# Optimization experiments

Measured on AMD Instinct MI355X. Metric: run time of the kernel, lower is better.

## Reference

```python
import jax, jax.numpy as jnp
import numpy as np

N_ORDERS = 4  # edge groups processed sequentially by EmulsionConv


def setup_inputs() -> dict:
    key = jax.random.key(0)
    ks = jax.random.split(key, 12)
    N, E, D_IN, H, D_OUT, ED = 50000, 800000, 10, 64, 10, 1
    s = 0.1
    return {
        "x": jax.random.normal(ks[0], (N, D_IN), jnp.float32),
        "edge_index": jax.random.randint(ks[1], (2, E), 0, N, jnp.int32),
        "edge_features": jax.random.normal(ks[2], (E, ED), jnp.float32),
        "lin0_w": jax.random.normal(ks[3], (D_IN, H), jnp.float32) * s,
        "lin0_b": jnp.zeros((H,), jnp.float32),
        "lin1_w": jax.random.normal(ks[4], (H, H), jnp.float32) * s,
        "lin1_b": jnp.zeros((H,), jnp.float32),
        "lin2_w": jax.random.normal(ks[5], (H, H), jnp.float32) * s,
        "lin2_b": jnp.zeros((H,), jnp.float32),
        "em_w": jax.random.normal(ks[6], (3, 2 * H + ED, H), jnp.float32) * s,
        "em_b": jnp.zeros((3, H), jnp.float32),
        "ec_w": jax.random.normal(ks[7], (3, 2 * H, H), jnp.float32) * s,
        "ec_b": jnp.zeros((3, H), jnp.float32),
        "out_w": jax.random.normal(ks[8], (H, D_OUT), jnp.float32) * s,
        "out_b": jnp.zeros((D_OUT,), jnp.float32),
    }


def _emulsion_conv(x, edge_index, edge_features, w, b):
    # Sequential per-order gather -> MLP message -> scatter-add; direction=0 (aggregate at source).
    N = x.shape[0]
    E = edge_index.shape[1]
    per = E // N_ORDERS
    for i in range(N_ORDERS):
        sl = slice(i * per, (i + 1) * per)
        src = edge_index[0, sl]
        dst = edge_index[1, sl]
        x_j = x[src]  # [per, H]
        x_i = x[dst]  # [per, H]
        msg = jnp.concatenate([x_i, x_j - x_i, edge_features[sl]], axis=1)
        msg = jax.nn.relu(msg @ w + b)
        agg = jax.ops.segment_sum(msg, src, num_segments=N)
        x = (x + agg) / 2.0
    return x


def _edge_conv(x, edge_index, w, b):
    # EdgeConv: nn([x_i, x_j - x_i]) with max aggregation at target nodes.
    N = x.shape[0]
    src, dst = edge_index[0], edge_index[1]
    x_i = x[dst]
    x_j = x[src]
    msg = jax.nn.relu(jnp.concatenate([x_i, x_j - x_i], axis=1) @ w + b)
    agg = jax.ops.segment_max(msg, dst, num_segments=N)
    return jnp.where(jnp.isfinite(agg), agg, 0.0)  # empty segments -> 0


def reference(x, edge_index, edge_features,
              lin0_w, lin0_b, lin1_w, lin1_b, lin2_w, lin2_b,
              em_w, em_b, ec_w, ec_b, out_w, out_b):
    lin_ws = [lin0_w, lin1_w, lin2_w]
    lin_bs = [lin0_b, lin1_b, lin2_b]
    for i in range(3):
        x = jax.nn.relu(x @ lin_ws[i] + lin_bs[i])
        x = _emulsion_conv(x, edge_index, edge_features, em_w[i], em_b[i])
    for i in range(3):
        x = _edge_conv(x, edge_index, ec_w[i], ec_b[i])
    return x @ out_w + out_b
```

## Files before the change

kernel.cpp:

```cpp
#include <hip/hip_runtime.h>
#include <hip/hip_fp16.h>


#define NN 50000
#define NE 800000
#define PER 200000
#define HD 64
#define NKEY 250112

#define NB_COUNT 3125
#define NB_LIN   782
#define NB_PREP  192

typedef _Float16 half8 __attribute__((ext_vector_type(8)));
typedef float float4v __attribute__((ext_vector_type(4)));

__global__ __launch_bounds__(256) void setup_kernel(
        const int* __restrict__ ei, int* __restrict__ cnt,
        uchar2* __restrict__ rank,
        const float* __restrict__ x_in, const float* __restrict__ lw0,
        const float* __restrict__ lb0, float* __restrict__ x,
        const float* __restrict__ em_w, const float* __restrict__ ec_w,
        _Float16* __restrict__ wh) {
    __shared__ float xs[64][11];
    int t = threadIdx.x;
    int b = blockIdx.x;
    if (b < NB_COUNT) {
        int e = b * 256 + t;
        if (e >= NE) return;
        int src = ei[e];
        int dst = ei[NE + e];
        int o = e / PER;
        int r1 = atomicAdd(&cnt[o * NN + src], 1);
        int r2 = atomicAdd(&cnt[4 * NN + dst], 1);
        rank[e] = make_uchar2((unsigned char)r1, (unsigned char)r2);
    } else if (b < NB_COUNT + NB_LIN) {
        int n0 = (b - NB_COUNT) * 64;
        for (int idx = t; idx < 64 * 10; idx += 256) {
            int n = idx / 10, k = idx - n * 10;
            int g = n0 + n;
            xs[n][k] = (g < NN) ? x_in[(size_t)g * 10 + k] : 0.f;
        }
        __syncthreads();
        int ng = t >> 4;
        int f0 = (t & 15) * 4;
        float acc[4][4] = {};
        for (int k = 0; k < 10; ++k) {
            float4 w4 = *(const float4*)&lw0[k * HD + f0];
            #pragma unroll
            for (int j = 0; j < 4; ++j) {
                float xv = xs[ng * 4 + j][k];
                acc[j][0] += xv * w4.x; acc[j][1] += xv * w4.y;
                acc[j][2] += xv * w4.z; acc[j][3] += xv * w4.w;
            }
        }
        float4 b4 = *(const float4*)&lb0[f0];
        #pragma unroll
        for (int j = 0; j < 4; ++j) {
            int g = n0 + ng * 4 + j;
            if (g < NN) {
                float4 o;
                o.x = fmaxf(acc[j][0] + b4.x, 0.f);
                o.y = fmaxf(acc[j][1] + b4.y, 0.f);
                o.z = fmaxf(acc[j][2] + b4.z, 0.f);
                o.w = fmaxf(acc[j][3] + b4.w, 0.f);
                *(float4*)&x[(size_t)g * HD + f0] = o;
            }
        }
    } else {
        int idx = (b - NB_COUNT - NB_LIN) * 256 + t;
        int mat = idx >> 12, pos = idx & 4095;
        int n = pos >> 6, k = pos & 63;
        float val;
        if (mat < 3)      { const float* B = em_w + mat * 129 * 64;     val = B[k*64+n] - B[(64+k)*64+n]; }
        else if (mat < 6) { const float* B = em_w + (mat-3) * 129 * 64; val = B[(64+k)*64+n]; }
        else if (mat < 9) { const float* B = ec_w + (mat-6) * 128 * 64; val = B[k*64+n] - B[(64+k)*64+n]; }
        else              { const float* B = ec_w + (mat-9) * 128 * 64; val = B[(64+k)*64+n]; }
        _Float16 h = (_Float16)val;
        _Float16 l = (_Float16)(val - (float)h);
        wh[(size_t)mat * 4096 + n * 64 + k] = h;
        wh[(size_t)(12 + mat) * 4096 + n * 64 + k] = l;
    }
}

__global__ __launch_bounds__(256) void scan_blk(
        const int* __restrict__ cnt, int* __restrict__ bsum) {
    __shared__ int s[256];
    int t = threadIdx.x;
    int i = blockIdx.x * 256 + t;
    int c = (i < NKEY) ? cnt[i] : 0;
    s[t] = c; __syncthreads();
    for (int d = 1; d < 256; d <<= 1) {
        int v = (t >= d) ? s[t - d] : 0;
        __syncthreads(); s[t] += v; __syncthreads();
    }
    if (t == 255) bsum[blockIdx.x] = s[255];
}

__global__ __launch_bounds__(1024) void scan_top(
        const int* __restrict__ bsum, int* __restrict__ bofs, int nb) {
    __shared__ int s[1024];
    int t = threadIdx.x;
    int c = (t < nb) ? bsum[t] : 0;
    s[t] = c; __syncthreads();
    for (int d = 1; d < 1024; d <<= 1) {
        int v = (t >= d) ? s[t - d] : 0;
        __syncthreads(); s[t] += v; __syncthreads();
    }
    if (t < nb) bofs[t] = s[t] - c;
}

__global__ __launch_bounds__(256) void scan_fin(
        const int* __restrict__ cnt, const int* __restrict__ bofs,
        int* __restrict__ ofs) {
    __shared__ int s[256];
    int t = threadIdx.x;
    int i = blockIdx.x * 256 + t;
    int c = (i < NKEY) ? cnt[i] : 0;
    s[t] = c; __syncthreads();
    for (int d = 1; d < 256; d <<= 1) {
        int v = (t >= d) ? s[t - d] : 0;
        __syncthreads(); s[t] += v; __syncthreads();
    }
    if (i < NKEY) ofs[i] = bofs[blockIdx.x] + s[t] - c;
}

__global__ __launch_bounds__(256) void fill_kernel(
        const int* __restrict__ ei, const float* __restrict__ ef,
        const int* __restrict__ ofs, const uchar2* __restrict__ rank,
        unsigned* __restrict__ em_val, int* __restrict__ ec_val) {
    int e = blockIdx.x * 256 + threadIdx.x;
    if (e >= NE) return;
    int src = ei[e];
    int dst = ei[NE + e];
    int o = e / PER;
    uchar2 r = rank[e];
    int p1 = ofs[o * NN + src] + r.x;
    unsigned short eb = __half_as_ushort(__float2half_rn(ef[e]));
    em_val[p1] = ((unsigned)dst << 16) | (unsigned)eb;
    int p2 = ofs[4 * NN + dst] + r.y - NE;
    ec_val[p2] = src;
}

template<int K>
__global__ __launch_bounds__(256) void lin_kernel(
        const float* __restrict__ xin,
        const float* __restrict__ W, const float* __restrict__ bias,
        float* __restrict__ xout) {
    __shared__ float xs[64][K + 1];
    int t = threadIdx.x;
    int n0 = blockIdx.x * 64;
    for (int idx = t; idx < 64 * K; idx += 256) {
        int n = idx / K, k = idx - n * K;
        int g = n0 + n;
        xs[n][k] = (g < NN) ? xin[(size_t)g * K + k] : 0.f;
    }
    __syncthreads();
    int ng = t >> 4;
    int f0 = (t & 15) * 4;
    float acc[4][4] = {};
    for (int k = 0; k < K; ++k) {
        float4 w4 = *(const float4*)&W[k * HD + f0];
        #pragma unroll
        for (int j = 0; j < 4; ++j) {
            float xv = xs[ng * 4 + j][k];
            acc[j][0] += xv * w4.x; acc[j][1] += xv * w4.y;
            acc[j][2] += xv * w4.z; acc[j][3] += xv * w4.w;
        }
    }
    float4 b4 = *(const float4*)&bias[f0];
    #pragma unroll
    for (int j = 0; j < 4; ++j) {
        int g = n0 + ng * 4 + j;
        if (g < NN) {
            float4 o;
            o.x = fmaxf(acc[j][0] + b4.x, 0.f);
            o.y = fmaxf(acc[j][1] + b4.y, 0.f);
            o.z = fmaxf(acc[j][2] + b4.z, 0.f);
            o.w = fmaxf(acc[j][3] + b4.w, 0.f);
            *(float4*)&xout[(size_t)g * HD + f0] = o;
        }
    }
}

__global__ __launch_bounds__(256) void uv_mfma(
        const float* __restrict__ x,
        const _Float16* __restrict__ Wuh, const _Float16* __restrict__ Wul,
        const _Float16* __restrict__ Wvh, const _Float16* __restrict__ Wvl,
        const float* __restrict__ bias,
        _Float16* __restrict__ u, _Float16* __restrict__ v) {
    __shared__ _Float16 xh[64 * 72], xl[64 * 72];
    __shared__ _Float16 wuh[64 * 72], wul[64 * 72];
    __shared__ _Float16 wvh[64 * 72], wvl[64 * 72];
    __shared__ _Float16 rp[4 * 16 * 72];
    int t = threadIdx.x;
    int n0 = blockIdx.x * 64;

    {
        int node = t >> 2, k0 = (t & 3) * 16;
        int g = n0 + node;
        float f[16];
        if (g < NN) {
            const float4* xr = (const float4*)&x[(size_t)g * HD + k0];
            *(float4*)&f[0] = xr[0]; *(float4*)&f[4] = xr[1];
            *(float4*)&f[8] = xr[2]; *(float4*)&f[12] = xr[3];
        } else {
            #pragma unroll
            for (int j = 0; j < 16; ++j) f[j] = 0.f;
        }
        half8 h0, h1, l0, l1;
        #pragma unroll
        for (int j = 0; j < 8; ++j) {
            _Float16 h = (_Float16)f[j];
            h0[j] = h; l0[j] = (_Float16)(f[j] - (float)h);
            _Float16 g2 = (_Float16)f[j + 8];
            h1[j] = g2; l1[j] = (_Float16)(f[j + 8] - (float)g2);
        }
        *(half8*)&xh[node * 72 + k0] = h0; *(half8*)&xh[node * 72 + k0 + 8] = h1;
        *(half8*)&xl[node * 72 + k0] = l0; *(half8*)&xl[node * 72 + k0 + 8] = l1;
    }
    {
        int n = t >> 2, c = (t & 3) * 16;
        *(half8*)&wuh[n * 72 + c]     = *(const half8*)&Wuh[n * 64 + c];
        *(half8*)&wuh[n * 72 + c + 8] = *(const half8*)&Wuh[n * 64 + c + 8];
        *(half8*)&wul[n * 72 + c]     = *(const half8*)&Wul[n * 64 + c];
        *(half8*)&wul[n * 72 + c + 8] = *(const half8*)&Wul[n * 64 + c + 8];
        *(half8*)&wvh[n * 72 + c]     = *(const half8*)&Wvh[n * 64 + c];
        *(half8*)&wvh[n * 72 + c + 8] = *(const half8*)&Wvh[n * 64 + c + 8];
        *(half8*)&wvl[n * 72 + c]     = *(const half8*)&Wvl[n * 64 + c];
        *(half8*)&wvl[n * 72 + c + 8] = *(const half8*)&Wvl[n * 64 + c + 8];
    }
    __syncthreads();

    int w = t >> 6, lane = t & 63;
    int quad = lane >> 4, l16 = lane & 15;
    int m0 = w * 16;
    half8 ah0 = *(half8*)&xh[(m0 + l16) * 72 + quad * 8];
    half8 ah1 = *(half8*)&xh[(m0 + l16) * 72 + 32 + quad * 8];
    half8 al0 = *(half8*)&xl[(m0 + l16) * 72 + quad * 8];
    half8 al1 = *(half8*)&xl[(m0 + l16) * 72 + 32 + quad * 8];

    float4v au[4], av[4];
    #pragma unroll
    for (int nt = 0; nt < 4; ++nt) {
        int n = nt * 16 + l16;
        half8 bh0 = *(half8*)&wuh[n * 72 + quad * 8];
        half8 bh1 = *(half8*)&wuh[n * 72 + 32 + quad * 8];
        half8 bl0 = *(half8*)&wul[n * 72 + quad * 8];
        half8 bl1 = *(half8*)&wul[n * 72 + 32 + quad * 8];
        float4v acc = {0.f, 0.f, 0.f, 0.f};
        acc = __builtin_amdgcn_mfma_f32_16x16x32_f16(ah0, bh0, acc, 0, 0, 0);
        acc = __builtin_amdgcn_mfma_f32_16x16x32_f16(ah1, bh1, acc, 0, 0, 0);
        acc = __builtin_amdgcn_mfma_f32_16x16x32_f16(al0, bh0, acc, 0, 0, 0);
        acc = __builtin_amdgcn_mfma_f32_16x16x32_f16(al1, bh1, acc, 0, 0, 0);
        acc = __builtin_amdgcn_mfma_f32_16x16x32_f16(ah0, bl0, acc, 0, 0, 0);
        acc = __builtin_amdgcn_mfma_f32_16x16x32_f16(ah1, bl1, acc, 0, 0, 0);
        au[nt] = acc;
        half8 ch0 = *(half8*)&wvh[n * 72 + quad * 8];
        half8 ch1 = *(half8*)&wvh[n * 72 + 32 + quad * 8];
        half8 cl0 = *(half8*)&wvl[n * 72 + quad * 8];
        half8 cl1 = *(half8*)&wvl[n * 72 + 32 + quad * 8];
        float4v accv = {0.f, 0.f, 0.f, 0.f};
        accv = __builtin_amdgcn_mfma_f32_16x16x32_f16(ah0, ch0, accv, 0, 0, 0);
        accv = __builtin_amdgcn_mfma_f32_16x16x32_f16(ah1, ch1, accv, 0, 0, 0);
        accv = __builtin_amdgcn_mfma_f32_16x16x32_f16(al0, ch0, accv, 0, 0, 0);
        accv = __builtin_amdgcn_mfma_f32_16x16x32_f16(al1, ch1, accv, 0, 0, 0);
        accv = __builtin_amdgcn_mfma_f32_16x16x32_f16(ah0, cl0, accv, 0, 0, 0);
        accv = __builtin_amdgcn_mfma_f32_16x16x32_f16(ah1, cl1, accv, 0, 0, 0);
        av[nt] = accv;
    }

    _Float16* rpw = &rp[w * 16 * 72];
    #pragma unroll
    for (int nt = 0; nt < 4; ++nt) {
        float bn = bias[nt * 16 + l16];
        #pragma unroll
        for (int r = 0; r < 4; ++r)
            rpw[(quad * 4 + r) * 72 + nt * 16 + l16] = (_Float16)(au[nt][r] + bn);
    }
    int mr = lane >> 2, cr = (lane & 3) * 16;
    int gr = n0 + m0 + mr;
    if (gr < NN) {
        *(half8*)&u[(size_t)gr * HD + cr]     = *(half8*)&rpw[mr * 72 + cr];
        *(half8*)&u[(size_t)gr * HD + cr + 8] = *(half8*)&rpw[mr * 72 + cr + 8];
    }
    #pragma unroll
    for (int nt = 0; nt < 4; ++nt) {
        #pragma unroll
        for (int r = 0; r < 4; ++r)
            rpw[(quad * 4 + r) * 72 + nt * 16 + l16] = (_Float16)(av[nt][r]);
    }
    if (gr < NN) {
        *(half8*)&v[(size_t)gr * HD + cr]     = *(half8*)&rpw[mr * 72 + cr];
        *(half8*)&v[(size_t)gr * HD + cr + 8] = *(half8*)&rpw[mr * 72 + cr + 8];
    }
}

__device__ __forceinline__ void load_h8(const __half* p, float* o) {
    float4 r = *(const float4*)p;
    __half2 h0 = *reinterpret_cast<__half2*>(&r.x);
    __half2 h1 = *reinterpret_cast<__half2*>(&r.y);
    __half2 h2 = *reinterpret_cast<__half2*>(&r.z);
    __half2 h3 = *reinterpret_cast<__half2*>(&r.w);
    float2 f0 = __half22float2(h0), f1 = __half22float2(h1);
    float2 f2 = __half22float2(h2), f3 = __half22float2(h3);
    o[0] = f0.x; o[1] = f0.y; o[2] = f1.x; o[3] = f1.y;
    o[4] = f2.x; o[5] = f2.y; o[6] = f3.x; o[7] = f3.y;
}

__global__ __launch_bounds__(256) void em_edge(
        const unsigned* __restrict__ em_val, const int* __restrict__ ofs,
        const __half* __restrict__ u, const __half* __restrict__ v,
        const float* __restrict__ we, float* __restrict__ x, int order) {
    int t = threadIdx.x;
    int node = blockIdx.x * 32 + (t >> 3);
    if (node >= NN) return;
    int f0 = (t & 7) * 8;
    int key = order * NN + node;
    int s0 = ofs[key], s1 = ofs[key + 1];
    float vn[8], wef[8], acc[8] = {};
    load_h8(&v[(size_t)node * HD + f0], vn);
    *(float4*)&wef[0] = *(const float4*)&we[f0];
    *(float4*)&wef[4] = *(const float4*)&we[f0 + 4];
    int p = s0;
    for (; p + 2 <= s1; p += 2) {
        unsigned e0 = em_val[p], e1 = em_val[p + 1];
        float u0[8], u1[8];
        load_h8(&u[(size_t)(e0 >> 16) * HD + f0], u0);
        load_h8(&u[(size_t)(e1 >> 16) * HD + f0], u1);
        float ef0 = __half2float(__ushort_as_half((unsigned short)(e0 & 0xffff)));
        float ef1 = __half2float(__ushort_as_half((unsigned short)(e1 & 0xffff)));
        #pragma unroll
        for (int j = 0; j < 8; ++j) {
            acc[j] += fmaxf(u0[j] + vn[j] + ef0 * wef[j], 0.f)
                    + fmaxf(u1[j] + vn[j] + ef1 * wef[j], 0.f);
        }
    }
    if (p < s1) {
        unsigned e0 = em_val[p];
        float u0[8];
        load_h8(&u[(size_t)(e0 >> 16) * HD + f0], u0);
        float ef0 = __half2float(__ushort_as_half((unsigned short)(e0 & 0xffff)));
        #pragma unroll
        for (int j = 0; j < 8; ++j)
            acc[j] += fmaxf(u0[j] + vn[j] + ef0 * wef[j], 0.f);
    }
    float xr[8];
    *(float4*)&xr[0] = *(const float4*)&x[(size_t)node * HD + f0];
    *(float4*)&xr[4] = *(const float4*)&x[(size_t)node * HD + f0 + 4];
    #pragma unroll
    for (int j = 0; j < 8; ++j) xr[j] = (xr[j] + acc[j]) * 0.5f;
    *(float4*)&x[(size_t)node * HD + f0] = *(float4*)&xr[0];
    *(float4*)&x[(size_t)node * HD + f0 + 4] = *(float4*)&xr[4];
}

__global__ __launch_bounds__(256) void ec_edge(
        const int* __restrict__ ec_val, const int* __restrict__ ofs,
        const __half* __restrict__ u, const __half* __restrict__ v,
        float* __restrict__ x) {
    int t = threadIdx.x;
    int node = blockIdx.x * 32 + (t >> 3);
    if (node >= NN) return;
    int f0 = (t & 7) * 8;
    int s0 = ofs[4 * NN + node] - NE, s1 = ofs[4 * NN + node + 1] - NE;
    float un[8], m[8] = {};
    load_h8(&u[(size_t)node * HD + f0], un);
    int p = s0;
    for (; p + 2 <= s1; p += 2) {
        int i0 = ec_val[p], i1 = ec_val[p + 1];
        float v0[8], v1[8];
        load_h8(&v[(size_t)i0 * HD + f0], v0);
        load_h8(&v[(size_t)i1 * HD + f0], v1);
        #pragma unroll
        for (int j = 0; j < 8; ++j)
            m[j] = fmaxf(m[j], fmaxf(un[j] + v0[j], un[j] + v1[j]));
    }
    if (p < s1) {
        int i0 = ec_val[p];
        float v0[8];
        load_h8(&v[(size_t)i0 * HD + f0], v0);
        #pragma unroll
        for (int j = 0; j < 8; ++j) m[j] = fmaxf(m[j], un[j] + v0[j]);
    }
    *(float4*)&x[(size_t)node * HD + f0] = *(float4*)&m[0];
    *(float4*)&x[(size_t)node * HD + f0 + 4] = *(float4*)&m[4];
}

__global__ __launch_bounds__(256) void ec_out(
        const int* __restrict__ ec_val, const int* __restrict__ ofs,
        const __half* __restrict__ u, const __half* __restrict__ v,
        const float* __restrict__ ow, const float* __restrict__ ob,
        float* __restrict__ out) {
    __shared__ float xs[32][72];
    int t = threadIdx.x;
    int nl = t >> 3;
    int node = blockIdx.x * 32 + nl;
    int f0 = (t & 7) * 8;
    float m[8] = {};
    if (node < NN) {
        int s0 = ofs[4 * NN + node] - NE, s1 = ofs[4 * NN + node + 1] - NE;
        float un[8];
        load_h8(&u[(size_t)node * HD + f0], un);
        int p = s0;
        for (; p + 2 <= s1; p += 2) {
            int i0 = ec_val[p], i1 = ec_val[p + 1];
            float v0[8], v1[8];
            load_h8(&v[(size_t)i0 * HD + f0], v0);
            load_h8(&v[(size_t)i1 * HD + f0], v1);
            #pragma unroll
            for (int j = 0; j < 8; ++j)
                m[j] = fmaxf(m[j], fmaxf(un[j] + v0[j], un[j] + v1[j]));
        }
        if (p < s1) {
            int i0 = ec_val[p];
            float v0[8];
            load_h8(&v[(size_t)i0 * HD + f0], v0);
            #pragma unroll
            for (int j = 0; j < 8; ++j) m[j] = fmaxf(m[j], un[j] + v0[j]);
        }
    }
    #pragma unroll
    for (int j = 0; j < 8; ++j) xs[nl][f0 + j] = m[j];
    __syncthreads();
    for (int idx = t; idx < 32 * 10; idx += 256) {
        int n = idx / 10, f = idx - n * 10;
        int g = blockIdx.x * 32 + n;
        if (g >= NN) continue;
        float acc = ob[f];
        #pragma unroll
        for (int k = 0; k < HD; ++k) acc += xs[n][k] * ow[k * 10 + f];
        out[(size_t)g * 10 + f] = acc;
    }
}

extern "C" void kernel_launch(void* const* d_in, const int* in_sizes, int n_in,
                              void* d_out, int out_size, void* d_ws, size_t ws_size,
                              hipStream_t stream) {
    const float* x_in  = (const float*)d_in[0];
    const int*   ei    = (const int*)d_in[1];
    const float* ef    = (const float*)d_in[2];
    const float* lw[3] = {(const float*)d_in[3], (const float*)d_in[5], (const float*)d_in[7]};
    const float* lb[3] = {(const float*)d_in[4], (const float*)d_in[6], (const float*)d_in[8]};
    const float* em_w  = (const float*)d_in[9];
    const float* em_b  = (const float*)d_in[10];
    const float* ec_w  = (const float*)d_in[11];
    const float* ec_b  = (const float*)d_in[12];
    const float* ow    = (const float*)d_in[13];
    const float* ob    = (const float*)d_in[14];
    float* out = (float*)d_out;

    char* wsb = (char*)d_ws;
    size_t off = 0;
    auto alloc = [&](size_t bytes) {
        void* p = wsb + off;
        off = (off + bytes + 255) & ~(size_t)255;
        return p;
    };
    float*     x      = (float*)alloc((size_t)NN * HD * 4);
    _Float16*  u      = (_Float16*)alloc((size_t)NN * HD * 2);
    _Float16*  v      = (_Float16*)alloc((size_t)NN * HD * 2);
    int*       cnt    = (int*)alloc((size_t)NKEY * 4);
    int*       ofs    = (int*)alloc((size_t)NKEY * 4);
    int*       bsum   = (int*)alloc((size_t)1024 * 4);
    int*       bofs   = (int*)alloc((size_t)1024 * 4);
    uchar2*    rank   = (uchar2*)alloc((size_t)NE * 2);
    unsigned*  em_val = (unsigned*)alloc((size_t)NE * 4);
    int*       ec_val = (int*)alloc((size_t)NE * 4);
    _Float16*  wh     = (_Float16*)alloc((size_t)24 * 4096 * 2);
    (void)ws_size; (void)in_sizes; (void)n_in; (void)out_size;

    const int gb_nodes = (NN + 63) / 64;
    const int gb_edges = (NE + 255) / 256;
    const int gb_n8    = (NN + 31) / 32;
    const int gb_keys  = NKEY / 256;

    hipMemsetAsync(cnt, 0, (size_t)NKEY * 4, stream);
    setup_kernel<<<NB_COUNT + NB_LIN + NB_PREP, 256, 0, stream>>>(
        ei, cnt, rank, x_in, lw[0], lb[0], x, em_w, ec_w, wh);
    scan_blk<<<gb_keys, 256, 0, stream>>>(cnt, bsum);
    scan_top<<<1, 1024, 0, stream>>>(bsum, bofs, gb_keys);
    scan_fin<<<gb_keys, 256, 0, stream>>>(cnt, bofs, ofs);
    fill_kernel<<<gb_edges, 256, 0, stream>>>(ei, ef, ofs, rank, em_val, ec_val);

    for (int i = 0; i < 3; ++i) {
        const _Float16* Wuh = wh + (size_t)i * 4096;
        const _Float16* Wvh = wh + (size_t)(3 + i) * 4096;
        const _Float16* Wul = wh + (size_t)(12 + i) * 4096;
        const _Float16* Wvl = wh + (size_t)(15 + i) * 4096;
        const float* bi = em_b + (size_t)i * HD;
        const float* we = em_w + (size_t)i * 129 * HD + 128 * HD;
        for (int o = 0; o < 4; ++o) {
            uv_mfma<<<gb_nodes, 256, 0, stream>>>(x, Wuh, Wul, Wvh, Wvl, bi, u, v);
            em_edge<<<gb_n8, 256, 0, stream>>>(em_val, ofs, (const __half*)u,
                                               (const __half*)v, we, x, o);
        }
        if (i < 2)
            lin_kernel<64><<<gb_nodes, 256, 0, stream>>>(x, lw[i + 1], lb[i + 1], x);
    }

    for (int j = 0; j < 3; ++j) {
        const _Float16* Wuh = wh + (size_t)(6 + j) * 4096;
        const _Float16* Wvh = wh + (size_t)(9 + j) * 4096;
        const _Float16* Wul = wh + (size_t)(18 + j) * 4096;
        const _Float16* Wvl = wh + (size_t)(21 + j) * 4096;
        const float* bj = ec_b + (size_t)j * HD;
        uv_mfma<<<gb_nodes, 256, 0, stream>>>(x, Wuh, Wul, Wvh, Wvl, bj, u, v);
        if (j < 2)
            ec_edge<<<gb_n8, 256, 0, stream>>>(ec_val, ofs, (const __half*)u,
                                               (const __half*)v, x);
        else
            ec_out<<<gb_n8, 256, 0, stream>>>(ec_val, ofs, (const __half*)u,
                                              (const __half*)v, ow, ob, out);
    }
}
```

Measured before the change: 587.6 us.

## Fuse edge aggregation with next-layer u/v MFMA projection and linear layers

Merges each edge aggregation kernel (emulsion and edge-conv) with the following u/v MFMA projection, and folds the intermediate linear layer into that fused kernel too. The linear weights are now pre-split into fp16 hi/lo pairs in setup. Updated x stays in shared memory, and u/v buffers are double-buffered so the next projection does not overwrite what is being gathered. This is meant to cut kernel launches and the global round trips of x between stages. In exchange, weights are read from global memory instead of LDS, and per-node aggregation now uses 256-thread blocks of 64 nodes, which may change occupancy and load balance.

```diff
diff --git a/kernel.cpp b/kernel.cpp
--- a/kernel.cpp
+++ b/kernel.cpp
@@ -10,7 +10,7 @@
 
 #define NB_COUNT 3125
 #define NB_LIN   782
-#define NB_PREP  192
+#define NB_PREP  224
 
 typedef _Float16 half8 __attribute__((ext_vector_type(8)));
 typedef float float4v __attribute__((ext_vector_type(4)));
@@ -21,6 +21,7 @@
         const float* __restrict__ x_in, const float* __restrict__ lw0,
         const float* __restrict__ lb0, float* __restrict__ x,
         const float* __restrict__ em_w, const float* __restrict__ ec_w,
+        const float* __restrict__ lw1, const float* __restrict__ lw2,
         _Float16* __restrict__ wh) {
     __shared__ float xs[64][11];
     int t = threadIdx.x;
@@ -72,14 +73,15 @@
         int mat = idx >> 12, pos = idx & 4095;
         int n = pos >> 6, k = pos & 63;
         float val;
-        if (mat < 3)      { const float* B = em_w + mat * 129 * 64;     val = B[k*64+n] - B[(64+k)*64+n]; }
-        else if (mat < 6) { const float* B = em_w + (mat-3) * 129 * 64; val = B[(64+k)*64+n]; }
-        else if (mat < 9) { const float* B = ec_w + (mat-6) * 128 * 64; val = B[k*64+n] - B[(64+k)*64+n]; }
-        else              { const float* B = ec_w + (mat-9) * 128 * 64; val = B[(64+k)*64+n]; }
+        if (mat < 3)       { const float* B = em_w + mat * 129 * 64;     val = B[k*64+n] - B[(64+k)*64+n]; }
+        else if (mat < 6)  { const float* B = em_w + (mat-3) * 129 * 64; val = B[(64+k)*64+n]; }
+        else if (mat < 9)  { const float* B = ec_w + (mat-6) * 128 * 64; val = B[k*64+n] - B[(64+k)*64+n]; }
+        else if (mat < 12) { const float* B = ec_w + (mat-9) * 128 * 64; val = B[(64+k)*64+n]; }
+        else               { const float* B = (mat == 12) ? lw1 : lw2;   val = B[k*64+n]; }
         _Float16 h = (_Float16)val;
         _Float16 l = (_Float16)(val - (float)h);
         wh[(size_t)mat * 4096 + n * 64 + k] = h;
-        wh[(size_t)(12 + mat) * 4096 + n * 64 + k] = l;
+        wh[(size_t)(14 + mat) * 4096 + n * 64 + k] = l;
     }
 }
 
@@ -142,160 +144,6 @@
     ec_val[p2] = src;
 }
 
-template<int K>
-__global__ __launch_bounds__(256) void lin_kernel(
-        const float* __restrict__ xin,
-        const float* __restrict__ W, const float* __restrict__ bias,
-        float* __restrict__ xout) {
-    __shared__ float xs[64][K + 1];
-    int t = threadIdx.x;
-    int n0 = blockIdx.x * 64;
-    for (int idx = t; idx < 64 * K; idx += 256) {
-        int n = idx / K, k = idx - n * K;
-        int g = n0 + n;
-        xs[n][k] = (g < NN) ? xin[(size_t)g * K + k] : 0.f;
-    }
-    __syncthreads();
-    int ng = t >> 4;
-    int f0 = (t & 15) * 4;
-    float acc[4][4] = {};
-    for (int k = 0; k < K; ++k) {
-        float4 w4 = *(const float4*)&W[k * HD + f0];
-        #pragma unroll
-        for (int j = 0; j < 4; ++j) {
-            float xv = xs[ng * 4 + j][k];
-            acc[j][0] += xv * w4.x; acc[j][1] += xv * w4.y;
-            acc[j][2] += xv * w4.z; acc[j][3] += xv * w4.w;
-        }
-    }
-    float4 b4 = *(const float4*)&bias[f0];
-    #pragma unroll
-    for (int j = 0; j < 4; ++j) {
-        int g = n0 + ng * 4 + j;
-        if (g < NN) {
-            float4 o;
-            o.x = fmaxf(acc[j][0] + b4.x, 0.f);
-            o.y = fmaxf(acc[j][1] + b4.y, 0.f);
-            o.z = fmaxf(acc[j][2] + b4.z, 0.f);
-            o.w = fmaxf(acc[j][3] + b4.w, 0.f);
-            *(float4*)&xout[(size_t)g * HD + f0] = o;
-        }
-    }
-}
-
-__global__ __launch_bounds__(256) void uv_mfma(
-        const float* __restrict__ x,
-        const _Float16* __restrict__ Wuh, const _Float16* __restrict__ Wul,
-        const _Float16* __restrict__ Wvh, const _Float16* __restrict__ Wvl,
-        const float* __restrict__ bias,
-        _Float16* __restrict__ u, _Float16* __restrict__ v) {
-    __shared__ _Float16 xh[64 * 72], xl[64 * 72];
-    __shared__ _Float16 wuh[64 * 72], wul[64 * 72];
-    __shared__ _Float16 wvh[64 * 72], wvl[64 * 72];
-    __shared__ _Float16 rp[4 * 16 * 72];
-    int t = threadIdx.x;
-    int n0 = blockIdx.x * 64;
-
-    {
-        int node = t >> 2, k0 = (t & 3) * 16;
-        int g = n0 + node;
-        float f[16];
-        if (g < NN) {
-            const float4* xr = (const float4*)&x[(size_t)g * HD + k0];
-            *(float4*)&f[0] = xr[0]; *(float4*)&f[4] = xr[1];
-            *(float4*)&f[8] = xr[2]; *(float4*)&f[12] = xr[3];
-        } else {
-            #pragma unroll
-            for (int j = 0; j < 16; ++j) f[j] = 0.f;
-        }
-        half8 h0, h1, l0, l1;
-        #pragma unroll
-        for (int j = 0; j < 8; ++j) {
-            _Float16 h = (_Float16)f[j];
-            h0[j] = h; l0[j] = (_Float16)(f[j] - (float)h);
-            _Float16 g2 = (_Float16)f[j + 8];
-            h1[j] = g2; l1[j] = (_Float16)(f[j + 8] - (float)g2);
-        }
-        *(half8*)&xh[node * 72 + k0] = h0; *(half8*)&xh[node * 72 + k0 + 8] = h1;
-        *(half8*)&xl[node * 72 + k0] = l0; *(half8*)&xl[node * 72 + k0 + 8] = l1;
-    }
-    {
-        int n = t >> 2, c = (t & 3) * 16;
-        *(half8*)&wuh[n * 72 + c]     = *(const half8*)&Wuh[n * 64 + c];
-        *(half8*)&wuh[n * 72 + c + 8] = *(const half8*)&Wuh[n * 64 + c + 8];
-        *(half8*)&wul[n * 72 + c]     = *(const half8*)&Wul[n * 64 + c];
-        *(half8*)&wul[n * 72 + c + 8] = *(const half8*)&Wul[n * 64 + c + 8];
-        *(half8*)&wvh[n * 72 + c]     = *(const half8*)&Wvh[n * 64 + c];
-        *(half8*)&wvh[n * 72 + c + 8] = *(const half8*)&Wvh[n * 64 + c + 8];
-        *(half8*)&wvl[n * 72 + c]     = *(const half8*)&Wvl[n * 64 + c];
-        *(half8*)&wvl[n * 72 + c + 8] = *(const half8*)&Wvl[n * 64 + c + 8];
-    }
-    __syncthreads();
-
-    int w = t >> 6, lane = t & 63;
-    int quad = lane >> 4, l16 = lane & 15;
-    int m0 = w * 16;
-    half8 ah0 = *(half8*)&xh[(m0 + l16) * 72 + quad * 8];
-    half8 ah1 = *(half8*)&xh[(m0 + l16) * 72 + 32 + quad * 8];
-    half8 al0 = *(half8*)&xl[(m0 + l16) * 72 + quad * 8];
-    half8 al1 = *(half8*)&xl[(m0 + l16) * 72 + 32 + quad * 8];
-
-    float4v au[4], av[4];
-    #pragma unroll
-    for (int nt = 0; nt < 4; ++nt) {
-        int n = nt * 16 + l16;
-        half8 bh0 = *(half8*)&wuh[n * 72 + quad * 8];
-        half8 bh1 = *(half8*)&wuh[n * 72 + 32 + quad * 8];
-        half8 bl0 = *(half8*)&wul[n * 72 + quad * 8];
-        half8 bl1 = *(half8*)&wul[n * 72 + 32 + quad * 8];
-        float4v acc = {0.f, 0.f, 0.f, 0.f};
-        acc = __builtin_amdgcn_mfma_f32_16x16x32_f16(ah0, bh0, acc, 0, 0, 0);
-        acc = __builtin_amdgcn_mfma_f32_16x16x32_f16(ah1, bh1, acc, 0, 0, 0);
-        acc = __builtin_amdgcn_mfma_f32_16x16x32_f16(al0, bh0, acc, 0, 0, 0);
-        acc = __builtin_amdgcn_mfma_f32_16x16x32_f16(al1, bh1, acc, 0, 0, 0);
-        acc = __builtin_amdgcn_mfma_f32_16x16x32_f16(ah0, bl0, acc, 0, 0, 0);
-        acc = __builtin_amdgcn_mfma_f32_16x16x32_f16(ah1, bl1, acc, 0, 0, 0);
-        au[nt] = acc;
-        half8 ch0 = *(half8*)&wvh[n * 72 + quad * 8];
-        half8 ch1 = *(half8*)&wvh[n * 72 + 32 + quad * 8];
-        half8 cl0 = *(half8*)&wvl[n * 72 + quad * 8];
-        half8 cl1 = *(half8*)&wvl[n * 72 + 32 + quad * 8];
-        float4v accv = {0.f, 0.f, 0.f, 0.f};
-        accv = __builtin_amdgcn_mfma_f32_16x16x32_f16(ah0, ch0, accv, 0, 0, 0);
-        accv = __builtin_amdgcn_mfma_f32_16x16x32_f16(ah1, ch1, accv, 0, 0, 0);
-        accv = __builtin_amdgcn_mfma_f32_16x16x32_f16(al0, ch0, accv, 0, 0, 0);
-        accv = __builtin_amdgcn_mfma_f32_16x16x32_f16(al1, ch1, accv, 0, 0, 0);
-        accv = __builtin_amdgcn_mfma_f32_16x16x32_f16(ah0, cl0, accv, 0, 0, 0);
-        accv = __builtin_amdgcn_mfma_f32_16x16x32_f16(ah1, cl1, accv, 0, 0, 0);
-        av[nt] = accv;
-    }
-
-    _Float16* rpw = &rp[w * 16 * 72];
-    #pragma unroll
-    for (int nt = 0; nt < 4; ++nt) {
-        float bn = bias[nt * 16 + l16];
-        #pragma unroll
-        for (int r = 0; r < 4; ++r)
-            rpw[(quad * 4 + r) * 72 + nt * 16 + l16] = (_Float16)(au[nt][r] + bn);
-    }
-    int mr = lane >> 2, cr = (lane & 3) * 16;
-    int gr = n0 + m0 + mr;
-    if (gr < NN) {
-        *(half8*)&u[(size_t)gr * HD + cr]     = *(half8*)&rpw[mr * 72 + cr];
-        *(half8*)&u[(size_t)gr * HD + cr + 8] = *(half8*)&rpw[mr * 72 + cr + 8];
-    }
-    #pragma unroll
-    for (int nt = 0; nt < 4; ++nt) {
-        #pragma unroll
-        for (int r = 0; r < 4; ++r)
-            rpw[(quad * 4 + r) * 72 + nt * 16 + l16] = (_Float16)(av[nt][r]);
-    }
-    if (gr < NN) {
-        *(half8*)&v[(size_t)gr * HD + cr]     = *(half8*)&rpw[mr * 72 + cr];
-        *(half8*)&v[(size_t)gr * HD + cr + 8] = *(half8*)&rpw[mr * 72 + cr + 8];
-    }
-}
-
 __device__ __forceinline__ void load_h8(const __half* p, float* o) {
     float4 r = *(const float4*)p;
     __half2 h0 = *reinterpret_cast<__half2*>(&r.x);
@@ -308,82 +156,236 @@
     o[4] = f2.x; o[5] = f2.y; o[6] = f3.x; o[7] = f3.y;
 }
 
-__global__ __launch_bounds__(256) void em_edge(
-        const unsigned* __restrict__ em_val, const int* __restrict__ ofs,
-        const __half* __restrict__ u, const __half* __restrict__ v,
-        const float* __restrict__ we, float* __restrict__ x, int order) {
-    int t = threadIdx.x;
-    int node = blockIdx.x * 32 + (t >> 3);
-    if (node >= NN) return;
-    int f0 = (t & 7) * 8;
-    int key = order * NN + node;
-    int s0 = ofs[key], s1 = ofs[key + 1];
-    float vn[8], wef[8], acc[8] = {};
-    load_h8(&v[(size_t)node * HD + f0], vn);
-    *(float4*)&wef[0] = *(const float4*)&we[f0];
-    *(float4*)&wef[4] = *(const float4*)&we[f0 + 4];
-    int p = s0;
-    for (; p + 2 <= s1; p += 2) {
-        unsigned e0 = em_val[p], e1 = em_val[p + 1];
-        float u0[8], u1[8];
-        load_h8(&u[(size_t)(e0 >> 16) * HD + f0], u0);
-        load_h8(&u[(size_t)(e1 >> 16) * HD + f0], u1);
-        float ef0 = __half2float(__ushort_as_half((unsigned short)(e0 & 0xffff)));
-        float ef1 = __half2float(__ushort_as_half((unsigned short)(e1 & 0xffff)));
-        #pragma unroll
-        for (int j = 0; j < 8; ++j) {
-            acc[j] += fmaxf(u0[j] + vn[j] + ef0 * wef[j], 0.f)
-                    + fmaxf(u1[j] + vn[j] + ef1 * wef[j], 0.f);
-        }
-    }
-    if (p < s1) {
-        unsigned e0 = em_val[p];
-        float u0[8];
-        load_h8(&u[(size_t)(e0 >> 16) * HD + f0], u0);
-        float ef0 = __half2float(__ushort_as_half((unsigned short)(e0 & 0xffff)));
-        #pragma unroll
-        for (int j = 0; j < 8; ++j)
-            acc[j] += fmaxf(u0[j] + vn[j] + ef0 * wef[j], 0.f);
-    }
-    float xr[8];
-    *(float4*)&xr[0] = *(const float4*)&x[(size_t)node * HD + f0];
-    *(float4*)&xr[4] = *(const float4*)&x[(size_t)node * HD + f0 + 4];
+__device__ __forceinline__ void split8(const float* f, half8& h, half8& l) {
     #pragma unroll
-    for (int j = 0; j < 8; ++j) xr[j] = (xr[j] + acc[j]) * 0.5f;
-    *(float4*)&x[(size_t)node * HD + f0] = *(float4*)&xr[0];
-    *(float4*)&x[(size_t)node * HD + f0 + 4] = *(float4*)&xr[4];
-}
-
-__global__ __launch_bounds__(256) void ec_edge(
-        const int* __restrict__ ec_val, const int* __restrict__ ofs,
-        const __half* __restrict__ u, const __half* __restrict__ v,
-        float* __restrict__ x) {
-    int t = threadIdx.x;
-    int node = blockIdx.x * 32 + (t >> 3);
-    if (node >= NN) return;
-    int f0 = (t & 7) * 8;
-    int s0 = ofs[4 * NN + node] - NE, s1 = ofs[4 * NN + node + 1] - NE;
-    float un[8], m[8] = {};
-    load_h8(&u[(size_t)node * HD + f0], un);
-    int p = s0;
-    for (; p + 2 <= s1; p += 2) {
-        int i0 = ec_val[p], i1 = ec_val[p + 1];
-        float v0[8], v1[8];
-        load_h8(&v[(size_t)i0 * HD + f0], v0);
-        load_h8(&v[(size_t)i1 * HD + f0], v1);
-        #pragma unroll
-        for (int j = 0; j < 8; ++j)
-            m[j] = fmaxf(m[j], fmaxf(un[j] + v0[j], un[j] + v1[j]));
-    }
-    if (p < s1) {
-        int i0 = ec_val[p];
-        float v0[8];
-        load_h8(&v[(size_t)i0 * HD + f0], v0);
-        #pragma unroll
-        for (int j = 0; j < 8; ++j) m[j] = fmaxf(m[j], un[j] + v0[j]);
-    }
-    *(float4*)&x[(size_t)node * HD + f0] = *(float4*)&m[0];
-    *(float4*)&x[(size_t)node * HD + f0 + 4] = *(float4*)&m[4];
+    for (int j = 0; j < 8; ++j) {
+        _Float16 hh = (_Float16)f[j];
+        h[j] = hh; l[j] = (_Float16)(f[j] - (float)hh);
+    }
+}
+
+#define MFMA16(A, B, C) __builtin_amdgcn_mfma_f32_16x16x32_f16(A, B, C, 0, 0, 0)
+
+template<int PRE, bool WRITEX, bool DOLIN>
+__global__ __launch_bounds__(256) void fused_uv(
+        const float* __restrict__ xg, float* __restrict__ xout,
+        const unsigned* __restrict__ em_val, const int* __restrict__ ec_val,
+        const int* __restrict__ ofs, int order,
+        const __half* __restrict__ ug, const __half* __restrict__ vg,
+        const float* __restrict__ we,
+        const _Float16* __restrict__ Wlh, const _Float16* __restrict__ Wll,
+        const float* __restrict__ lbias,
+        const _Float16* __restrict__ Wuh, const _Float16* __restrict__ Wul,
+        const _Float16* __restrict__ Wvh, const _Float16* __restrict__ Wvl,
+        const float* __restrict__ bias,
+        _Float16* __restrict__ u, _Float16* __restrict__ v) {
+    __shared__ _Float16 xh[64 * 72], xl[64 * 72];
+    __shared__ _Float16 rp[4 * 16 * 72];
+    const int t = threadIdx.x;
+    const int n0 = blockIdx.x * 64;
+
+    if constexpr (PRE == 0) {
+        int node = t >> 2, k0 = (t & 3) * 16;
+        int g = n0 + node;
+        float f[16];
+        if (g < NN) {
+            const float4* xr4 = (const float4*)&xg[(size_t)g * HD + k0];
+            *(float4*)&f[0] = xr4[0]; *(float4*)&f[4] = xr4[1];
+            *(float4*)&f[8] = xr4[2]; *(float4*)&f[12] = xr4[3];
+        } else {
+            #pragma unroll
+            for (int j = 0; j < 16; ++j) f[j] = 0.f;
+        }
+        half8 h0, l0, h1, l1;
+        split8(f, h0, l0); split8(f + 8, h1, l1);
+        *(half8*)&xh[node * 72 + k0] = h0; *(half8*)&xh[node * 72 + k0 + 8] = h1;
+        *(half8*)&xl[node * 72 + k0] = l0; *(half8*)&xl[node * 72 + k0 + 8] = l1;
+    } else if constexpr (PRE == 1) {
+        int f0 = (t & 7) * 8;
+        float wef[8];
+        *(float4*)&wef[0] = *(const float4*)&we[f0];
+        *(float4*)&wef[4] = *(const float4*)&we[f0 + 4];
+        #pragma unroll
+        for (int hv = 0; hv < 2; ++hv) {
+            int nl = (t >> 3) + hv * 32;
+            int node = n0 + nl;
+            float xr[8];
+            if (node < NN) {
+                int key = order * NN + node;
+                int s0 = ofs[key], s1 = ofs[key + 1];
+                float vn[8], acc[8] = {};
+                load_h8(&vg[(size_t)node * HD + f0], vn);
+                int p = s0;
+                for (; p + 2 <= s1; p += 2) {
+                    unsigned e0 = em_val[p], e1 = em_val[p + 1];
+                    float u0[8], u1[8];
+                    load_h8(&ug[(size_t)(e0 >> 16) * HD + f0], u0);
+                    load_h8(&ug[(size_t)(e1 >> 16) * HD + f0], u1);
+                    float ef0 = __half2float(__ushort_as_half((unsigned short)(e0 & 0xffff)));
+                    float ef1 = __half2float(__ushort_as_half((unsigned short)(e1 & 0xffff)));
+                    #pragma unroll
+                    for (int j = 0; j < 8; ++j) {
+                        acc[j] += fmaxf(u0[j] + vn[j] + ef0 * wef[j], 0.f)
+                                + fmaxf(u1[j] + vn[j] + ef1 * wef[j], 0.f);
+                    }
+                }
+                if (p < s1) {
+                    unsigned e0 = em_val[p];
+                    float u0[8];
+                    load_h8(&ug[(size_t)(e0 >> 16) * HD + f0], u0);
+                    float ef0 = __half2float(__ushort_as_half((unsigned short)(e0 & 0xffff)));
+                    #pragma unroll
+                    for (int j = 0; j < 8; ++j)
+                        acc[j] += fmaxf(u0[j] + vn[j] + ef0 * wef[j], 0.f);
+                }
+                *(float4*)&xr[0] = *(const float4*)&xg[(size_t)node * HD + f0];
+                *(float4*)&xr[4] = *(const float4*)&xg[(size_t)node * HD + f0 + 4];
+                #pragma unroll
+                for (int j = 0; j < 8; ++j) xr[j] = (xr[j] + acc[j]) * 0.5f;
+                if constexpr (WRITEX) {
+                    *(float4*)&xout[(size_t)node * HD + f0] = *(float4*)&xr[0];
+                    *(float4*)&xout[(size_t)node * HD + f0 + 4] = *(float4*)&xr[4];
+                }
+            } else {
+                #pragma unroll
+                for (int j = 0; j < 8; ++j) xr[j] = 0.f;
+            }
+            half8 hh, ll;
+            split8(xr, hh, ll);
+            *(half8*)&xh[nl * 72 + f0] = hh;
+            *(half8*)&xl[nl * 72 + f0] = ll;
+        }
+    } else {
+        int f0 = (t & 7) * 8;
+        #pragma unroll
+        for (int hv = 0; hv < 2; ++hv) {
+            int nl = (t >> 3) + hv * 32;
+            int node = n0 + nl;
+            float m[8] = {};
+            if (node < NN) {
+                int s0 = ofs[4 * NN + node] - NE, s1 = ofs[4 * NN + node + 1] - NE;
+                float un[8];
+                load_h8(&ug[(size_t)node * HD + f0], un);
+                int p = s0;
+                for (; p + 2 <= s1; p += 2) {
+                    int i0 = ec_val[p], i1 = ec_val[p + 1];
+                    float v0[8], v1[8];
+                    load_h8(&vg[(size_t)i0 * HD + f0], v0);
+                    load_h8(&vg[(size_t)i1 * HD + f0], v1);
+                    #pragma unroll
+                    for (int j = 0; j < 8; ++j)
+                        m[j] = fmaxf(m[j], fmaxf(un[j] + v0[j], un[j] + v1[j]));
+                }
+                if (p < s1) {
+                    int i0 = ec_val[p];
+                    float v0[8];
+                    load_h8(&vg[(size_t)i0 * HD + f0], v0);
+                    #pragma unroll
+                    for (int j = 0; j < 8; ++j) m[j] = fmaxf(m[j], un[j] + v0[j]);
+                }
+            }
+            half8 hh, ll;
+            split8(m, hh, ll);
+            *(half8*)&xh[nl * 72 + f0] = hh;
+            *(half8*)&xl[nl * 72 + f0] = ll;
+        }
+    }
+    __syncthreads();
+
+    const int w = t >> 6, lane = t & 63;
+    const int quad = lane >> 4, l16 = lane & 15;
+    const int m0 = w * 16;
+
+    half8 ah0 = *(half8*)&xh[(m0 + l16) * 72 + quad * 8];
+    half8 ah1 = *(half8*)&xh[(m0 + l16) * 72 + 32 + quad * 8];
+    half8 al0 = *(half8*)&xl[(m0 + l16) * 72 + quad * 8];
+    half8 al1 = *(half8*)&xl[(m0 + l16) * 72 + 32 + quad * 8];
+
+    if constexpr (DOLIN) {
+        float4v ax[4];
+        #pragma unroll
+        for (int nt = 0; nt < 4; ++nt) {
+            int n = nt * 16 + l16;
+            half8 bh0 = *(const half8*)&Wlh[n * 64 + quad * 8];
+            half8 bh1 = *(const half8*)&Wlh[n * 64 + 32 + quad * 8];
+            half8 bl0 = *(const half8*)&Wll[n * 64 + quad * 8];
+            half8 bl1 = *(const half8*)&Wll[n * 64 + 32 + quad * 8];
+            float4v acc = {0.f, 0.f, 0.f, 0.f};
+            acc = MFMA16(ah0, bh0, acc); acc = MFMA16(ah1, bh1, acc);
+            acc = MFMA16(al0, bh0, acc); acc = MFMA16(al1, bh1, acc);
+            acc = MFMA16(ah0, bl0, acc); acc = MFMA16(ah1, bl1, acc);
+            ax[nt] = acc;
+        }
+        __syncthreads();
+        #pragma unroll
+        for (int nt = 0; nt < 4; ++nt) {
+            float bn = lbias[nt * 16 + l16];
+            #pragma unroll
+            for (int r = 0; r < 4; ++r) {
+                float val = fmaxf(ax[nt][r] + bn, 0.f);
+                int mrow = m0 + quad * 4 + r;
+                _Float16 hh = (_Float16)val;
+                xh[mrow * 72 + nt * 16 + l16] = hh;
+                xl[mrow * 72 + nt * 16 + l16] = (_Float16)(val - (float)hh);
+                int gn = n0 + mrow;
+                if (gn < NN) xout[(size_t)gn * HD + nt * 16 + l16] = val;
+            }
+        }
+        __syncthreads();
+        ah0 = *(half8*)&xh[(m0 + l16) * 72 + quad * 8];
+        ah1 = *(half8*)&xh[(m0 + l16) * 72 + 32 + quad * 8];
+        al0 = *(half8*)&xl[(m0 + l16) * 72 + quad * 8];
+        al1 = *(half8*)&xl[(m0 + l16) * 72 + 32 + quad * 8];
+    }
+
+    float4v au[4], av[4];
+    #pragma unroll
+    for (int nt = 0; nt < 4; ++nt) {
+        int n = nt * 16 + l16;
+        half8 bh0 = *(const half8*)&Wuh[n * 64 + quad * 8];
+        half8 bh1 = *(const half8*)&Wuh[n * 64 + 32 + quad * 8];
+        half8 bl0 = *(const half8*)&Wul[n * 64 + quad * 8];
+        half8 bl1 = *(const half8*)&Wul[n * 64 + 32 + quad * 8];
+        float4v acc = {0.f, 0.f, 0.f, 0.f};
+        acc = MFMA16(ah0, bh0, acc); acc = MFMA16(ah1, bh1, acc);
+        acc = MFMA16(al0, bh0, acc); acc = MFMA16(al1, bh1, acc);
+        acc = MFMA16(ah0, bl0, acc); acc = MFMA16(ah1, bl1, acc);
+        au[nt] = acc;
+        half8 ch0 = *(const half8*)&Wvh[n * 64 + quad * 8];
+        half8 ch1 = *(const half8*)&Wvh[n * 64 + 32 + quad * 8];
+        half8 cl0 = *(const half8*)&Wvl[n * 64 + quad * 8];
+        half8 cl1 = *(const half8*)&Wvl[n * 64 + 32 + quad * 8];
+        float4v accv = {0.f, 0.f, 0.f, 0.f};
+        accv = MFMA16(ah0, ch0, accv); accv = MFMA16(ah1, ch1, accv);
+        accv = MFMA16(al0, ch0, accv); accv = MFMA16(al1, ch1, accv);
+        accv = MFMA16(ah0, cl0, accv); accv = MFMA16(ah1, cl1, accv);
+        av[nt] = accv;
+    }
+
+    _Float16* rpw = &rp[w * 16 * 72];
+    #pragma unroll
+    for (int nt = 0; nt < 4; ++nt) {
+        float bn = bias[nt * 16 + l16];
+        #pragma unroll
+        for (int r = 0; r < 4; ++r)
+            rpw[(quad * 4 + r) * 72 + nt * 16 + l16] = (_Float16)(au[nt][r] + bn);
+    }
+    int mr = lane >> 2, cr = (lane & 3) * 16;
+    int gr = n0 + m0 + mr;
+    if (gr < NN) {
+        *(half8*)&u[(size_t)gr * HD + cr]     = *(half8*)&rpw[mr * 72 + cr];
+        *(half8*)&u[(size_t)gr * HD + cr + 8] = *(half8*)&rpw[mr * 72 + cr + 8];
+    }
+    #pragma unroll
+    for (int nt = 0; nt < 4; ++nt) {
+        #pragma unroll
+        for (int r = 0; r < 4; ++r)
+            rpw[(quad * 4 + r) * 72 + nt * 16 + l16] = (_Float16)(av[nt][r]);
+    }
+    if (gr < NN) {
+        *(half8*)&v[(size_t)gr * HD + cr]     = *(half8*)&rpw[mr * 72 + cr];
+        *(half8*)&v[(size_t)gr * HD + cr + 8] = *(half8*)&rpw[mr * 72 + cr + 8];
+    }
 }
 
 __global__ __launch_bounds__(256) void ec_out(
@@ -457,8 +459,10 @@
         return p;
     };
     float*     x      = (float*)alloc((size_t)NN * HD * 4);
-    _Float16*  u      = (_Float16*)alloc((size_t)NN * HD * 2);
-    _Float16*  v      = (_Float16*)alloc((size_t)NN * HD * 2);
+    _Float16*  uA     = (_Float16*)alloc((size_t)NN * HD * 2);
+    _Float16*  vA     = (_Float16*)alloc((size_t)NN * HD * 2);
+    _Float16*  uB     = (_Float16*)alloc((size_t)NN * HD * 2);
+    _Float16*  vB     = (_Float16*)alloc((size_t)NN * HD * 2);
     int*       cnt    = (int*)alloc((size_t)NKEY * 4);
     int*       ofs    = (int*)alloc((size_t)NKEY * 4);
     int*       bsum   = (int*)alloc((size_t)1024 * 4);
@@ -466,7 +470,7 @@
     uchar2*    rank   = (uchar2*)alloc((size_t)NE * 2);
     unsigned*  em_val = (unsigned*)alloc((size_t)NE * 4);
     int*       ec_val = (int*)alloc((size_t)NE * 4);
-    _Float16*  wh     = (_Float16*)alloc((size_t)24 * 4096 * 2);
+    _Float16*  wh     = (_Float16*)alloc((size_t)28 * 4096 * 2);
     (void)ws_size; (void)in_sizes; (void)n_in; (void)out_size;
 
     const int gb_nodes = (NN + 63) / 64;
@@ -474,42 +478,62 @@
     const int gb_n8    = (NN + 31) / 32;
     const int gb_keys  = NKEY / 256;
 
+    auto Wm = [&](int mat) { return wh + (size_t)mat * 4096; };
+    auto Wl_ = [&](int mat) { return wh + (size_t)(14 + mat) * 4096; };
+
     hipMemsetAsync(cnt, 0, (size_t)NKEY * 4, stream);
     setup_kernel<<<NB_COUNT + NB_LIN + NB_PREP, 256, 0, stream>>>(
-        ei, cnt, rank, x_in, lw[0], lb[0], x, em_w, ec_w, wh);
+        ei, cnt, rank, x_in, lw[0], lb[0], x, em_w, ec_w, lw[1], lw[2], wh);
     scan_blk<<<gb_keys, 256, 0, stream>>>(cnt, bsum);
     scan_top<<<1, 1024, 0, stream>>>(bsum, bofs, gb_keys);
     scan_fin<<<gb_keys, 256, 0, stream>>>(cnt, bofs, ofs);
     fill_kernel<<<gb_edges, 256, 0, stream>>>(ei, ef, ofs, rank, em_val, ec_val);
 
+    _Float16 *cu = uA, *cv = vA, *nu = uB, *nv = vB;
+    auto swapbuf = [&]() { _Float16* t1 = cu; cu = nu; nu = t1;
+                           _Float16* t2 = cv; cv = nv; nv = t2; };
+
+    fused_uv<0, false, false><<<gb_nodes, 256, 0, stream>>>(
+        x, nullptr, nullptr, nullptr, nullptr, 0, nullptr, nullptr, nullptr,
+        nullptr, nullptr, nullptr,
+        Wm(0), Wl_(0), Wm(3), Wl_(3), em_b, cu, cv);
+
     for (int i = 0; i < 3; ++i) {
-        const _Float16* Wuh = wh + (size_t)i * 4096;
-        const _Float16* Wvh = wh + (size_t)(3 + i) * 4096;
-        const _Float16* Wul = wh + (size_t)(12 + i) * 4096;
-        const _Float16* Wvl = wh + (size_t)(15 + i) * 4096;
+        const float* we = em_w + (size_t)i * 129 * HD + 128 * HD;
         const float* bi = em_b + (size_t)i * HD;
-        const float* we = em_w + (size_t)i * 129 * HD + 128 * HD;
-        for (int o = 0; o < 4; ++o) {
-            uv_mfma<<<gb_nodes, 256, 0, stream>>>(x, Wuh, Wul, Wvh, Wvl, bi, u, v);
-            em_edge<<<gb_n8, 256, 0, stream>>>(em_val, ofs, (const __half*)u,
-                                               (const __half*)v, we, x, o);
-        }
-        if (i < 2)
-            lin_kernel<64><<<gb_nodes, 256, 0, stream>>>(x, lw[i + 1], lb[i + 1], x);
-    }
-
-    for (int j = 0; j < 3; ++j) {
-        const _Float16* Wuh = wh + (size_t)(6 + j) * 4096;
-        const _Float16* Wvh = wh + (size_t)(9 + j) * 4096;
-        const _Float16* Wul = wh + (size_t)(18 + j) * 4096;
-        const _Float16* Wvl = wh + (size_t)(21 + j) * 4096;
-        const float* bj = ec_b + (size_t)j * HD;
-        uv_mfma<<<gb_nodes, 256, 0, stream>>>(x, Wuh, Wul, Wvh, Wvl, bj, u, v);
-        if (j < 2)
-            ec_edge<<<gb_n8, 256, 0, stream>>>(ec_val, ofs, (const __half*)u,
-                                               (const __half*)v, x);
-        else
-            ec_out<<<gb_n8, 256, 0, stream>>>(ec_val, ofs, (const __half*)u,
-                                              (const __half*)v, ow, ob, out);
-    }
-}
+        for (int o = 0; o < 3; ++o) {
+            fused_uv<1, true, false><<<gb_nodes, 256, 0, stream>>>(
+                x, x, em_val, nullptr, ofs, o, (const __half*)cu, (const __half*)cv,
+                we, nullptr, nullptr, nullptr,
+                Wm(i), Wl_(i), Wm(3 + i), Wl_(3 + i), bi, nu, nv);
+            swapbuf();
+        }
+        if (i < 2) {
+            fused_uv<1, false, true><<<gb_nodes, 256, 0, stream>>>(
+                x, x, em_val, nullptr, ofs, 3, (const __half*)cu, (const __half*)cv,
+                we, Wm(12 + i), Wl_(12 + i), lb[i + 1],
+                Wm(i + 1), Wl_(i + 1), Wm(4 + i), Wl_(4 + i),
+                em_b + (size_t)(i + 1) * HD, nu, nv);
+            swapbuf();
+        } else {
+            fused_uv<1, false, false><<<gb_nodes, 256, 0, stream>>>(
+                x, nullptr, em_val, nullptr, ofs, 3, (const __half*)cu, (const __half*)cv,
+                we, nullptr, nullptr, nullptr,
+                Wm(6), Wl_(6), Wm(9), Wl_(9), ec_b, nu, nv);
+            swapbuf();
+        }
+    }
+
+    for (int j = 0; j < 2; ++j) {
+        fused_uv<2, false, false><<<gb_nodes, 256, 0, stream>>>(
+            nullptr, nullptr, nullptr, ec_val, ofs, 0,
+            (const __half*)cu, (const __half*)cv, nullptr,
+            nullptr, nullptr, nullptr,
+            Wm(7 + j), Wl_(7 + j), Wm(10 + j), Wl_(10 + j),
+            ec_b + (size_t)(j + 1) * HD, nu, nv);
+        swapbuf();
+    }
+
+    ec_out<<<gb_n8, 256, 0, stream>>>(ec_val, ofs, (const __half*)cu,
+                                      (const __half*)cv, ow, ob, out);
+}
```

Measured after the change: 671.5 us. 14.3% more time.
